# Performance work log

Measured on AMD Instinct MI355X. Metric: run time of the kernel, lower is better.

The kernel has to match this reference:

```python
import jax, jax.numpy as jnp
import numpy as np

B, L, D_MODEL = 4, 2048, 256
D_STATE, D_CONV, EXPAND = 16, 4, 2
D_INNER = EXPAND * D_MODEL          # 512
DT_RANK = (D_MODEL + 15) // 16      # 16
HORIZON = 96


def setup_inputs() -> dict:
    key = jax.random.key(0)
    ks = jax.random.split(key, 8)
    s = lambda k, shape, scale=0.02: jax.random.normal(k, shape, dtype=jnp.float32) * scale
    return {
        "x": jax.random.normal(ks[0], (B, L, D_MODEL), dtype=jnp.float32),
        "in_proj_w": s(ks[1], (2 * D_INNER, D_MODEL)),          # no bias (mamba default)
        "conv_w": s(ks[2], (D_INNER, 1, D_CONV), 0.1),          # depthwise causal conv
        "conv_b": jnp.zeros((D_INNER,), jnp.float32),
        "x_proj_w": s(ks[3], (DT_RANK + 2 * D_STATE, D_INNER)),
        "dt_proj_w": s(ks[4], (D_INNER, DT_RANK), 0.1),
        # softplus^{-1}(0.01): typical small initial dt
        "dt_proj_b": jnp.log(jnp.expm1(jnp.full((D_INNER,), 0.01, jnp.float32))),
        "A_log": jnp.log(jnp.broadcast_to(jnp.arange(1, D_STATE + 1, dtype=jnp.float32), (D_INNER, D_STATE))),
        "D_param": jnp.ones((D_INNER,), jnp.float32),
        "out_proj_w": s(ks[5], (D_MODEL, D_INNER)),
        "head_w": s(ks[6], (HORIZON, D_MODEL)),
        "head_b": jnp.zeros((HORIZON,), jnp.float32),
    }


def _silu(x):
    return x * jax.nn.sigmoid(x)


def _forward(x, in_proj_w, conv_w, conv_b, x_proj_w, dt_proj_w, dt_proj_b,
             A_log, D_param, out_proj_w, head_w, head_b):
    # in_proj -> split into conv/ssm branch and gate z
    xz = x @ in_proj_w.T                      # (B, L, 2*d_inner)
    x_in, z = jnp.split(xz, 2, axis=-1)
    # depthwise causal conv over time
    x_t = jnp.transpose(x_in, (0, 2, 1))      # (B, d_inner, L)
    x_conv = jax.lax.conv_general_dilated(
        x_t, conv_w, (1,), [(D_CONV - 1, 0)],
        feature_group_count=D_INNER, dimension_numbers=("NCH", "OIH", "NCH"))
    u = _silu(jnp.transpose(x_conv + conv_b[None, :, None], (0, 2, 1)))  # (B, L, d_inner)
    # input-dependent dt, B, C
    x_dbl = u @ x_proj_w.T
    dt, Bm, Cm = jnp.split(x_dbl, [DT_RANK, DT_RANK + D_STATE], axis=-1)
    delta = jax.nn.softplus(dt @ dt_proj_w.T + dt_proj_b)  # (B, L, d_inner)
    A = -jnp.exp(A_log)                                     # (d_inner, d_state)
    deltaA = jnp.exp(delta[..., None] * A)                  # (B, L, d_inner, d_state)
    deltaBu = delta[..., None] * Bm[:, :, None, :] * u[..., None]

    def step(h, ins):
        dA, dBu, c = ins                                    # (B,d,n),(B,d,n),(B,n)
        h = dA * h + dBu
        y = jnp.einsum("bdn,bn->bd", h, c)
        return h, y

    h0 = jnp.zeros((x.shape[0], D_INNER, D_STATE), x.dtype)
    xs = (jnp.moveaxis(deltaA, 1, 0), jnp.moveaxis(deltaBu, 1, 0), jnp.moveaxis(Cm, 1, 0))
    _, ys = jax.lax.scan(step, h0, xs)                      # (L, B, d_inner)
    y = jnp.moveaxis(ys, 0, 1) + u * D_param
    y = y * _silu(z)
    out = y @ out_proj_w.T                                  # (B, L, d_model)
    last = out[:, -1, :]
    return last @ head_w.T + head_b                         # (B, HORIZON)


def reference(x, in_proj_w, conv_w, conv_b, x_proj_w, dt_proj_w, dt_proj_b,
              A_log, D_param, out_proj_w, head_w, head_b):
    return _forward(x, in_proj_w, conv_w, conv_b, x_proj_w, dt_proj_w, dt_proj_b,
                    A_log, D_param, out_proj_w, head_w, head_b)
```

## Files before the change

kernel.cpp:

```cpp
#include <hip/hip_runtime.h>
#include <math.h>

#define BATCH 4
#define LSEQ 2048
#define BL (BATCH*LSEQ)
#define DMODEL 256
#define DINNER 512
#define NSTATE 16
#define DTRANK 16
#define NPROJ 48
#define HORIZ 96
#define NCH 32
#define TCH (LSEQ/NCH)

typedef __attribute__((ext_vector_type(8))) short short8b;
typedef __attribute__((ext_vector_type(4))) float f32x4;

__device__ __forceinline__ unsigned short f2bf(float f) {
  unsigned u = __float_as_uint(f);
  u += 0x7FFF + ((u >> 16) & 1);
  return (unsigned short)(u >> 16);
}

__global__ __launch_bounds__(256) void k_inproj(const float* __restrict__ X,
                                                const float* __restrict__ W,
                                                float* __restrict__ xinT) {
  __shared__ unsigned short sA[128][40];
  __shared__ unsigned short sB[128][40];
  const int m0 = blockIdx.x * 128;
  const int j0 = blockIdx.y * 128;
  const int tid = threadIdx.x;
  const int lane = tid & 63;
  const int wave = tid >> 6;
  const int jw = (wave & 1) * 64;
  const int mw = (wave >> 1) * 64;
  const int r  = tid >> 1;
  const int kh = (tid & 1) * 16;
  const int fl = lane & 15;
  const int fg = lane >> 4;
  const float* Asrc = &W[(size_t)(j0 + r) * DMODEL + kh];
  const float* Bsrc = &X[(size_t)(m0 + r) * DMODEL + kh];
  f32x4 acc[4][4];
  #pragma unroll
  for (int f = 0; f < 4; ++f)
    #pragma unroll
    for (int g = 0; g < 4; ++g) acc[f][g] = (f32x4){0.f, 0.f, 0.f, 0.f};
  float4 av[4], bv[4];
  #pragma unroll
  for (int q = 0; q < 4; ++q) {
    av[q] = *(const float4*)(Asrc + 4 * q);
    bv[q] = *(const float4*)(Bsrc + 4 * q);
  }
  for (int kb = 0; kb < DMODEL; kb += 32) {
    __syncthreads();
    {
      unsigned short ta[16], tb[16];
      #pragma unroll
      for (int q = 0; q < 4; ++q) {
        ta[4*q+0]=f2bf(av[q].x); ta[4*q+1]=f2bf(av[q].y); ta[4*q+2]=f2bf(av[q].z); ta[4*q+3]=f2bf(av[q].w);
        tb[4*q+0]=f2bf(bv[q].x); tb[4*q+1]=f2bf(bv[q].y); tb[4*q+2]=f2bf(bv[q].z); tb[4*q+3]=f2bf(bv[q].w);
      }
      *(short8b*)&sA[r][kh]     = *(short8b*)&ta[0];
      *(short8b*)&sA[r][kh + 8] = *(short8b*)&ta[8];
      *(short8b*)&sB[r][kh]     = *(short8b*)&tb[0];
      *(short8b*)&sB[r][kh + 8] = *(short8b*)&tb[8];
    }
    __syncthreads();
    if (kb + 32 < DMODEL) {
      #pragma unroll
      for (int q = 0; q < 4; ++q) {
        av[q] = *(const float4*)(Asrc + kb + 32 + 4 * q);
        bv[q] = *(const float4*)(Bsrc + kb + 32 + 4 * q);
      }
    }
    short8b af[4], bf[4];
    #pragma unroll
    for (int f = 0; f < 4; ++f) {
      af[f] = *(const short8b*)&sA[jw + f * 16 + fl][fg * 8];
      bf[f] = *(const short8b*)&sB[mw + f * 16 + fl][fg * 8];
    }
    #pragma unroll
    for (int f = 0; f < 4; ++f)
      #pragma unroll
      for (int g = 0; g < 4; ++g)
        acc[f][g] = __builtin_amdgcn_mfma_f32_16x16x32_bf16(af[f], bf[g], acc[f][g], 0, 0, 0);
  }
  #pragma unroll
  for (int f = 0; f < 4; ++f) {
    const int j = j0 + jw + f * 16 + fg * 4;
    #pragma unroll
    for (int g = 0; g < 4; ++g) {
      const int m = m0 + mw + g * 16 + fl;
      #pragma unroll
      for (int rg = 0; rg < 4; ++rg)
        xinT[(size_t)(j + rg) * BL + m] = acc[f][g][rg];
    }
  }
}

__global__ __launch_bounds__(256) void k_convdbl(const float* __restrict__ xinT,
                                                 const float* __restrict__ cw,
                                                 const float* __restrict__ cb,
                                                 const float* __restrict__ xpw,
                                                 const float* __restrict__ opw,
                                                 const float* __restrict__ hw,
                                                 float* __restrict__ uT,
                                                 float* __restrict__ dbl,
                                                 float* __restrict__ hwf) {
  __shared__ float sw2[48][132];
  __shared__ float su[128][33];
  const int btc = blockIdx.x;
  const int tid = threadIdx.x;
  if (btc >= 256) {
    const int fid = btc - 256;
    const int k0 = fid * 8;
    const int kk = tid & 7;
    const int t0 = tid >> 3;
    float* scratch = &sw2[0][0];
    for (int i = tid; i < 512; i += 256) {
      int m = i >> 1, half = (i & 1) << 2;
      *(float4*)&scratch[m * 8 + half] = *(const float4*)&opw[(size_t)m * DINNER + k0 + half];
    }
    __syncthreads();
    #pragma unroll
    for (int tb = 0; tb < 3; ++tb) {
      int t = tb * 32 + t0;
      const float* hr = &hw[(size_t)t * DMODEL];
      float acc = 0.f;
      #pragma unroll 8
      for (int m = 0; m < DMODEL; ++m) acc = fmaf(hr[m], scratch[m * 8 + kk], acc);
      hwf[(size_t)t * DINNER + k0 + kk] = acc;
    }
    return;
  }
  const int bt0 = btc * 32;
  const bool edge0 = ((bt0 & (LSEQ - 1)) == 0);
  const int t0 = (tid & 15) << 1;
  const int o0 = (tid >> 4) * 3;
  const int cr = tid >> 1;
  const int cc = (tid & 1) << 4;
  float acc[2][3] = {};
  for (int kp = 0; kp < 4; ++kp) {
    const int kbase = kp * 128;
    __syncthreads();
    #pragma unroll
    for (int q = 0; q < 6; ++q) {
      int idx = tid + q * 256;
      int o = idx >> 5, k4 = (idx & 31) << 2;
      *(float4*)&sw2[o][k4] = *(const float4*)&xpw[(size_t)o * DINNER + kbase + k4];
    }
    {
      const int d = kbase + cr;
      const float* xr = &xinT[(size_t)d * BL + bt0 + cc];
      float4 v0 = *(const float4*)xr;
      float4 v1 = *(const float4*)(xr + 4);
      float4 v2 = *(const float4*)(xr + 8);
      float4 v3 = *(const float4*)(xr + 12);
      bool edge = edge0 && (cc == 0);
      float p1, p2, p3;
      if (edge) { p1 = p2 = p3 = 0.f; }
      else { p1 = xr[-3]; p2 = xr[-2]; p3 = xr[-1]; }
      float4 wv = *(const float4*)&cw[d * 4];
      float bias = cb[d];
      float xv[19] = {p1, p2, p3, v0.x, v0.y, v0.z, v0.w, v1.x, v1.y, v1.z, v1.w,
                      v2.x, v2.y, v2.z, v2.w, v3.x, v3.y, v3.z, v3.w};
      float uu[16];
      #pragma unroll
      for (int c = 0; c < 16; ++c) {
        float s = bias;
        s = fmaf(wv.x, xv[c],     s);
        s = fmaf(wv.y, xv[c + 1], s);
        s = fmaf(wv.z, xv[c + 2], s);
        s = fmaf(wv.w, xv[c + 3], s);
        uu[c] = s / (1.f + __expf(-s));
      }
      #pragma unroll
      for (int q = 0; q < 4; ++q) {
        float4 w4 = make_float4(uu[4*q], uu[4*q+1], uu[4*q+2], uu[4*q+3]);
        *(float4*)&su[cr][cc + 4*q] = w4;
        *(float4*)&uT[(size_t)d * BL + bt0 + cc + 4*q] = w4;
      }
    }
    __syncthreads();
    #pragma unroll 4
    for (int kk = 0; kk < 128; ++kk) {
      float2 uv = *(const float2*)&su[kk][t0];
      float w0 = sw2[o0][kk], w1 = sw2[o0 + 1][kk], w2 = sw2[o0 + 2][kk];
      acc[0][0] = fmaf(uv.x, w0, acc[0][0]);
      acc[0][1] = fmaf(uv.x, w1, acc[0][1]);
      acc[0][2] = fmaf(uv.x, w2, acc[0][2]);
      acc[1][0] = fmaf(uv.y, w0, acc[1][0]);
      acc[1][1] = fmaf(uv.y, w1, acc[1][1]);
      acc[1][2] = fmaf(uv.y, w2, acc[1][2]);
    }
  }
  #pragma unroll
  for (int i = 0; i < 2; ++i)
    #pragma unroll
    for (int j = 0; j < 3; ++j)
      dbl[(size_t)(bt0 + t0 + i) * NPROJ + o0 + j] = acc[i][j];
}

__global__ __launch_bounds__(256) void k_scan(const float* __restrict__ uT,
                                              const float* __restrict__ dbl,
                                              const float* __restrict__ dtw,
                                              const float* __restrict__ dtb,
                                              const float* __restrict__ Alog,
                                              float* __restrict__ aprod,
                                              float* __restrict__ hacc) {
  __shared__ float sdt[64][17];
  __shared__ float sB[64][16];
  __shared__ float sdp[16][66][2];
  __shared__ float su[16][68];
  __shared__ float sdtw[16][17];
  __shared__ float sdtb[16];
  const int dblk = blockIdx.x, c = blockIdx.y, b = blockIdx.z;
  const int tid = threadIdx.x;
  const int d0 = dblk * 16;
  const int bt0 = b * LSEQ + c * TCH;
  {
    int tok = tid >> 2, q = (tid & 3) << 2;
    float4 v = *(const float4*)&dbl[(size_t)(bt0 + tok) * NPROJ + q];
    sdt[tok][q] = v.x; sdt[tok][q + 1] = v.y; sdt[tok][q + 2] = v.z; sdt[tok][q + 3] = v.w;
    float4 w = *(const float4*)&dbl[(size_t)(bt0 + tok) * NPROJ + DTRANK + q];
    *(float4*)&sB[tok][q] = w;
    int dl = tid >> 4, tq = (tid & 15) << 2;
    *(float4*)&su[dl][tq] = *(const float4*)&uT[(size_t)(d0 + dl) * BL + bt0 + tq];
    sdtw[tid >> 4][tid & 15] = dtw[(d0 + (tid >> 4)) * DTRANK + (tid & 15)];
    if (tid < 16) sdtb[tid] = dtb[d0 + tid];
  }
  __syncthreads();
  {
    int tok = tid >> 2, dl4 = (tid & 3) << 2;
    #pragma unroll
    for (int dd = 0; dd < 4; ++dd) {
      int dl = dl4 + dd;
      float a = sdtb[dl];
      #pragma unroll
      for (int r = 0; r < DTRANK; ++r) a = fmaf(sdt[tok][r], sdtw[dl][r], a);
      float dlt = (a > 20.f) ? a : log1pf(__expf(a));
      sdp[dl][tok][0] = dlt;
      sdp[dl][tok][1] = dlt * su[dl][tok];
    }
  }
  __syncthreads();
  const int dl = tid >> 4, n = tid & 15;
  const int d = d0 + dl;
  const float A = -__expf(Alog[d * NSTATE + n]);
  float ap = 1.f, h = 0.f;
  #pragma unroll 8
  for (int tt = 0; tt < TCH; ++tt) {
    float2 dp = *(const float2*)&sdp[dl][tt][0];
    float dA = __expf(dp.x * A);
    h = fmaf(dA, h, dp.y * sB[tt][n]);
    ap *= dA;
  }
  size_t off = (((size_t)b * NCH + c) * DINNER + d) * NSTATE + n;
  aprod[off] = ap;
  hacc[off] = h;
}

__global__ __launch_bounds__(256) void k_combine(const float* __restrict__ aprod,
                                                 const float* __restrict__ hacc,
                                                 const float* __restrict__ dbl,
                                                 const float* __restrict__ uT,
                                                 const float* __restrict__ Dp,
                                                 const float* __restrict__ X,
                                                 const float* __restrict__ ipw,
                                                 float* __restrict__ ybuf) {
  __shared__ float sx[DMODEL];
  const int dblk = blockIdx.x & 31, b = blockIdx.x >> 5;
  const int tid = threadIdx.x;
  const int dl = tid >> 4, n = tid & 15;
  const int d = dblk * 16 + dl;
  sx[tid] = X[((size_t)b * LSEQ + LSEQ - 1) * DMODEL + tid];
  float h = 0.f;
  for (int c = 0; c < NCH; ++c) {
    size_t off = (((size_t)b * NCH + c) * DINNER + d) * NSTATE + n;
    h = fmaf(aprod[off], h, hacc[off]);
  }
  __syncthreads();
  float zp = 0.f;
  {
    const float* zr = &ipw[(size_t)(DINNER + d) * DMODEL + (n << 4)];
    #pragma unroll
    for (int q = 0; q < 4; ++q) {
      float4 w4 = *(const float4*)&zr[q << 2];
      float4 x4 = *(const float4*)&sx[(n << 4) + (q << 2)];
      zp = fmaf(w4.x, x4.x, zp); zp = fmaf(w4.y, x4.y, zp);
      zp = fmaf(w4.z, x4.z, zp); zp = fmaf(w4.w, x4.w, zp);
    }
  }
  const int btL = b * LSEQ + LSEQ - 1;
  float Cv = dbl[(size_t)btL * NPROJ + DTRANK + NSTATE + n];
  float v = h * Cv;
  #pragma unroll
  for (int off = 1; off < 16; off <<= 1) {
    v  += __shfl_xor(v, off);
    zp += __shfl_xor(zp, off);
  }
  if (n == 0) {
    float y = v + uT[(size_t)d * BL + btL] * Dp[d];
    ybuf[b * DINNER + d] = y * zp / (1.f + __expf(-zp));
  }
}

__global__ __launch_bounds__(256) void k_out(const float* __restrict__ sy,
                                             const float* __restrict__ hwf,
                                             const float* __restrict__ hb,
                                             float* __restrict__ out) {
  const int t = blockIdx.x;
  const int b = threadIdx.x >> 6;
  const int lane = threadIdx.x & 63;
  const int k0 = lane << 3;
  const float* yr = &sy[(size_t)b * DINNER + k0];
  const float* wr = &hwf[(size_t)t * DINNER + k0];
  float4 y0 = *(const float4*)yr, y1 = *(const float4*)(yr + 4);
  float4 w0 = *(const float4*)wr, w1 = *(const float4*)(wr + 4);
  float s = y0.x * w0.x + y0.y * w0.y + y0.z * w0.z + y0.w * w0.w
          + y1.x * w1.x + y1.y * w1.y + y1.z * w1.z + y1.w * w1.w;
  #pragma unroll
  for (int off = 1; off < 64; off <<= 1) s += __shfl_xor(s, off);
  if (lane == 0) out[b * HORIZ + t] = s + hb[t];
}

extern "C" void kernel_launch(void* const* d_in, const int* in_sizes, int n_in,
                              void* d_out, int out_size, void* d_ws, size_t ws_size,
                              hipStream_t stream) {
  (void)in_sizes; (void)n_in; (void)out_size; (void)ws_size;
  const float* x    = (const float*)d_in[0];
  const float* ipw  = (const float*)d_in[1];
  const float* cw   = (const float*)d_in[2];
  const float* cb   = (const float*)d_in[3];
  const float* xpw  = (const float*)d_in[4];
  const float* dtw  = (const float*)d_in[5];
  const float* dtb  = (const float*)d_in[6];
  const float* Alog = (const float*)d_in[7];
  const float* Dp   = (const float*)d_in[8];
  const float* opw  = (const float*)d_in[9];
  const float* hw   = (const float*)d_in[10];
  const float* hb   = (const float*)d_in[11];
  float* out = (float*)d_out;
  float* ws  = (float*)d_ws;

  float* xinT  = ws;
  float* uT    = ws + 4194304;
  float* dbl   = ws + 8388608;
  float* aprod = ws + 8781824;
  float* hacc  = ws + 9830400;
  float* ybuf  = ws + 10878976;
  float* hwf   = ws + 10881024;

  k_inproj<<<dim3(64, 4), 256, 0, stream>>>(x, ipw, xinT);
  k_convdbl<<<320, 256, 0, stream>>>(xinT, cw, cb, xpw, opw, hw, uT, dbl, hwf);
  k_scan<<<dim3(32, NCH, BATCH), 256, 0, stream>>>(uT, dbl, dtw, dtb, Alog, aprod, hacc);
  k_combine<<<128, 256, 0, stream>>>(aprod, hacc, dbl, uT, Dp, x, ipw, ybuf);
  k_out<<<HORIZ, 256, 0, stream>>>(ybuf, hwf, hb, out);
}
```

Measured before the change: 77.02 us.

## Fuse in_proj GEMM with causal conv and x_proj into one front kernel

Merges the in_proj MFMA GEMM and the conv/SiLU/x_proj kernel into a single kernel. Each block computes the x_in slice for its 32 tokens plus a 16-token halo in registers, applies the depthwise causal conv through lane shuffles, and feeds u straight into the x_proj product. This removes the xinT round trip through global memory and one launch. The cost is redundant halo GEMM work per block, a double-buffered bf16 weight staging loop that syncs every k-step, and x_proj weights now rounded to bf16.

```diff
diff --git a/kernel.cpp b/kernel.cpp
--- a/kernel.cpp
+++ b/kernel.cpp
@@ -14,6 +14,7 @@
 #define TCH (LSEQ/NCH)
 
 typedef __attribute__((ext_vector_type(8))) short short8b;
+typedef __attribute__((ext_vector_type(4))) short short4b;
 typedef __attribute__((ext_vector_type(4))) float f32x4;
 
 __device__ __forceinline__ unsigned short f2bf(float f) {
@@ -21,184 +22,175 @@
   u += 0x7FFF + ((u >> 16) & 1);
   return (unsigned short)(u >> 16);
 }
-
-__global__ __launch_bounds__(256) void k_inproj(const float* __restrict__ X,
-                                                const float* __restrict__ W,
-                                                float* __restrict__ xinT) {
-  __shared__ unsigned short sA[128][40];
-  __shared__ unsigned short sB[128][40];
-  const int m0 = blockIdx.x * 128;
-  const int j0 = blockIdx.y * 128;
+__device__ __forceinline__ float bf2f(unsigned short h) {
+  return __uint_as_float(((unsigned)h) << 16);
+}
+
+__global__ __launch_bounds__(512) void k_front(const float* __restrict__ X,
+                                               const float* __restrict__ W,
+                                               const float* __restrict__ cw,
+                                               const float* __restrict__ cb,
+                                               const float* __restrict__ xpw,
+                                               const float* __restrict__ opw,
+                                               const float* __restrict__ hw,
+                                               float* __restrict__ uT,
+                                               float* __restrict__ dbl,
+                                               float* __restrict__ hwf) {
+  __shared__ unsigned short sBX[32*48*8];
+  __shared__ unsigned short sAW[2*4*128*8];
+  __shared__ float u_lds[128*36];
   const int tid = threadIdx.x;
-  const int lane = tid & 63;
-  const int wave = tid >> 6;
-  const int jw = (wave & 1) * 64;
-  const int mw = (wave >> 1) * 64;
-  const int r  = tid >> 1;
-  const int kh = (tid & 1) * 16;
-  const int fl = lane & 15;
-  const int fg = lane >> 4;
-  const float* Asrc = &W[(size_t)(j0 + r) * DMODEL + kh];
-  const float* Bsrc = &X[(size_t)(m0 + r) * DMODEL + kh];
-  f32x4 acc[4][4];
-  #pragma unroll
-  for (int f = 0; f < 4; ++f)
-    #pragma unroll
-    for (int g = 0; g < 4; ++g) acc[f][g] = (f32x4){0.f, 0.f, 0.f, 0.f};
-  float4 av[4], bv[4];
-  #pragma unroll
-  for (int q = 0; q < 4; ++q) {
-    av[q] = *(const float4*)(Asrc + 4 * q);
-    bv[q] = *(const float4*)(Bsrc + 4 * q);
-  }
-  for (int kb = 0; kb < DMODEL; kb += 32) {
-    __syncthreads();
-    {
-      unsigned short ta[16], tb[16];
-      #pragma unroll
-      for (int q = 0; q < 4; ++q) {
-        ta[4*q+0]=f2bf(av[q].x); ta[4*q+1]=f2bf(av[q].y); ta[4*q+2]=f2bf(av[q].z); ta[4*q+3]=f2bf(av[q].w);
-        tb[4*q+0]=f2bf(bv[q].x); tb[4*q+1]=f2bf(bv[q].y); tb[4*q+2]=f2bf(bv[q].z); tb[4*q+3]=f2bf(bv[q].w);
-      }
-      *(short8b*)&sA[r][kh]     = *(short8b*)&ta[0];
-      *(short8b*)&sA[r][kh + 8] = *(short8b*)&ta[8];
-      *(short8b*)&sB[r][kh]     = *(short8b*)&tb[0];
-      *(short8b*)&sB[r][kh + 8] = *(short8b*)&tb[8];
-    }
-    __syncthreads();
-    if (kb + 32 < DMODEL) {
-      #pragma unroll
-      for (int q = 0; q < 4; ++q) {
-        av[q] = *(const float4*)(Asrc + kb + 32 + 4 * q);
-        bv[q] = *(const float4*)(Bsrc + kb + 32 + 4 * q);
-      }
-    }
-    short8b af[4], bf[4];
-    #pragma unroll
-    for (int f = 0; f < 4; ++f) {
-      af[f] = *(const short8b*)&sA[jw + f * 16 + fl][fg * 8];
-      bf[f] = *(const short8b*)&sB[mw + f * 16 + fl][fg * 8];
-    }
-    #pragma unroll
-    for (int f = 0; f < 4; ++f)
-      #pragma unroll
-      for (int g = 0; g < 4; ++g)
-        acc[f][g] = __builtin_amdgcn_mfma_f32_16x16x32_bf16(af[f], bf[g], acc[f][g], 0, 0, 0);
-  }
-  #pragma unroll
-  for (int f = 0; f < 4; ++f) {
-    const int j = j0 + jw + f * 16 + fg * 4;
-    #pragma unroll
-    for (int g = 0; g < 4; ++g) {
-      const int m = m0 + mw + g * 16 + fl;
-      #pragma unroll
-      for (int rg = 0; rg < 4; ++rg)
-        xinT[(size_t)(j + rg) * BL + m] = acc[f][g][rg];
-    }
-  }
-}
-
-__global__ __launch_bounds__(256) void k_convdbl(const float* __restrict__ xinT,
-                                                 const float* __restrict__ cw,
-                                                 const float* __restrict__ cb,
-                                                 const float* __restrict__ xpw,
-                                                 const float* __restrict__ opw,
-                                                 const float* __restrict__ hw,
-                                                 float* __restrict__ uT,
-                                                 float* __restrict__ dbl,
-                                                 float* __restrict__ hwf) {
-  __shared__ float sw2[48][132];
-  __shared__ float su[128][33];
   const int btc = blockIdx.x;
-  const int tid = threadIdx.x;
   if (btc >= 256) {
     const int fid = btc - 256;
     const int k0 = fid * 8;
-    const int kk = tid & 7;
-    const int t0 = tid >> 3;
-    float* scratch = &sw2[0][0];
-    for (int i = tid; i < 512; i += 256) {
-      int m = i >> 1, half = (i & 1) << 2;
-      *(float4*)&scratch[m * 8 + half] = *(const float4*)&opw[(size_t)m * DINNER + k0 + half];
-    }
-    __syncthreads();
-    #pragma unroll
-    for (int tb = 0; tb < 3; ++tb) {
-      int t = tb * 32 + t0;
+    float* scratch = u_lds;
+    {
+      int m = tid >> 1;
+      int half = (tid & 1) << 2;
+      *(float4*)&scratch[m * 8 + half] =
+        *(const float4*)&opw[(size_t)m * DINNER + k0 + half];
+    }
+    __syncthreads();
+    for (int u = tid; u < HORIZ * 8; u += 512) {
+      int t = u >> 3, kk = u & 7;
       const float* hr = &hw[(size_t)t * DMODEL];
       float acc = 0.f;
       #pragma unroll 8
-      for (int m = 0; m < DMODEL; ++m) acc = fmaf(hr[m], scratch[m * 8 + kk], acc);
+      for (int m = 0; m < DMODEL; ++m) acc = fmaf(hr[m], scratch[m*8 + kk], acc);
       hwf[(size_t)t * DINNER + k0 + kk] = acc;
     }
     return;
   }
   const int bt0 = btc * 32;
   const bool edge0 = ((bt0 & (LSEQ - 1)) == 0);
-  const int t0 = (tid & 15) << 1;
-  const int o0 = (tid >> 4) * 3;
-  const int cr = tid >> 1;
-  const int cc = (tid & 1) << 4;
-  float acc[2][3] = {};
-  for (int kp = 0; kp < 4; ++kp) {
-    const int kbase = kp * 128;
-    __syncthreads();
+  const int lane = tid & 63;
+  const int w  = tid >> 6;
+  const int fl = lane & 15;
+  const int fg = lane >> 4;
+  for (int u = tid; u < 1536; u += 512) {
+    int tok = u >> 5, ko = u & 31;
+    int g = bt0 - 16 + tok;
+    if (g < 0) g = 0;
+    const float* xr = &X[(size_t)g * DMODEL + ko * 8];
+    float4 a = *(const float4*)xr, b = *(const float4*)(xr + 4);
+    unsigned short t8[8] = {f2bf(a.x), f2bf(a.y), f2bf(a.z), f2bf(a.w),
+                            f2bf(b.x), f2bf(b.y), f2bf(b.z), f2bf(b.w)};
+    *(short8b*)&sBX[(ko * 48 + tok) * 8] = *(short8b*)t8;
+  }
+  float facc[4] = {0.f, 0.f, 0.f, 0.f};
+  const int xo = tid >> 3;
+  const int xt = (tid & 7) * 4;
+  const int sj = tid >> 2;
+  const int sk = tid & 3;
+  for (int jc = 0; jc < 4; ++jc) {
+    const int jbase = jc * 128;
+    __syncthreads();
+    {
+      const float* wr = &W[(size_t)(jbase + sj) * DMODEL + sk * 8];
+      float4 a = *(const float4*)wr, b = *(const float4*)(wr + 4);
+      unsigned short t8[8] = {f2bf(a.x), f2bf(a.y), f2bf(a.z), f2bf(a.w),
+                              f2bf(b.x), f2bf(b.y), f2bf(b.z), f2bf(b.w)};
+      *(short8b*)&sAW[(sk * 128 + sj) * 8] = *(short8b*)t8;
+    }
+    __syncthreads();
+    f32x4 acc0 = {0,0,0,0}, acc1 = {0,0,0,0}, acc2 = {0,0,0,0};
+    for (int ks = 0; ks < 8; ++ks) {
+      const int buf = ks & 1;
+      if (ks < 7) {
+        const float* wr = &W[(size_t)(jbase + sj) * DMODEL + (ks + 1) * 32 + sk * 8];
+        float4 a = *(const float4*)wr, b = *(const float4*)(wr + 4);
+        unsigned short t8[8] = {f2bf(a.x), f2bf(a.y), f2bf(a.z), f2bf(a.w),
+                                f2bf(b.x), f2bf(b.y), f2bf(b.z), f2bf(b.w)};
+        *(short8b*)&sAW[((buf ^ 1) * 512 + sk * 128 + sj) * 8] = *(short8b*)t8;
+      }
+      short8b aw = *(short8b*)&sAW[(buf * 512 + fg * 128 + w * 16 + fl) * 8];
+      short8b x0 = *(short8b*)&sBX[((ks * 4 + fg) * 48 + fl) * 8];
+      short8b x1 = *(short8b*)&sBX[((ks * 4 + fg) * 48 + 16 + fl) * 8];
+      short8b x2 = *(short8b*)&sBX[((ks * 4 + fg) * 48 + 32 + fl) * 8];
+      acc0 = __builtin_amdgcn_mfma_f32_16x16x32_bf16(x0, aw, acc0, 0, 0, 0);
+      acc1 = __builtin_amdgcn_mfma_f32_16x16x32_bf16(x1, aw, acc1, 0, 0, 0);
+      acc2 = __builtin_amdgcn_mfma_f32_16x16x32_bf16(x2, aw, acc2, 0, 0, 0);
+      __syncthreads();
+    }
+    if (edge0) acc0 = (f32x4){0,0,0,0};
+    const int j = jbase + w * 16 + fl;
+    const float4 cwv = *(const float4*)&cw[j * 4];
+    const float cbv = cb[j];
+    float u1[4], u2[4];
+    {
+      float s3a = __shfl(acc1[3], lane - 16), s3b = __shfl(acc0[3], lane + 48);
+      float s2a = __shfl(acc1[2], lane - 16), s2b = __shfl(acc0[2], lane + 48);
+      float s1a = __shfl(acc1[1], lane - 16), s1b = __shfl(acc0[1], lane + 48);
+      float p1 = fg ? s3a : s3b, p2 = fg ? s2a : s2b, p3 = fg ? s1a : s1b;
+      float xm1[4] = {p1, acc1[0], acc1[1], acc1[2]};
+      float xm2[4] = {p2, p1, acc1[0], acc1[1]};
+      float xm3[4] = {p3, p2, p1, acc1[0]};
+      #pragma unroll
+      for (int r = 0; r < 4; ++r) {
+        float s = cbv;
+        s = fmaf(cwv.x, xm3[r], s); s = fmaf(cwv.y, xm2[r], s);
+        s = fmaf(cwv.z, xm1[r], s); s = fmaf(cwv.w, acc1[r], s);
+        u1[r] = s / (1.f + __expf(-s));
+      }
+    }
+    {
+      float s3a = __shfl(acc2[3], lane - 16), s3b = __shfl(acc1[3], lane + 48);
+      float s2a = __shfl(acc2[2], lane - 16), s2b = __shfl(acc1[2], lane + 48);
+      float s1a = __shfl(acc2[1], lane - 16), s1b = __shfl(acc1[1], lane + 48);
+      float p1 = fg ? s3a : s3b, p2 = fg ? s2a : s2b, p3 = fg ? s1a : s1b;
+      float xm1[4] = {p1, acc2[0], acc2[1], acc2[2]};
+      float xm2[4] = {p2, p1, acc2[0], acc2[1]};
+      float xm3[4] = {p3, p2, p1, acc2[0]};
+      #pragma unroll
+      for (int r = 0; r < 4; ++r) {
+        float s = cbv;
+        s = fmaf(cwv.x, xm3[r], s); s = fmaf(cwv.y, xm2[r], s);
+        s = fmaf(cwv.z, xm1[r], s); s = fmaf(cwv.w, acc2[r], s);
+        u2[r] = s / (1.f + __expf(-s));
+      }
+    }
+    {
+      const int jl = w * 16 + fl;
+      #pragma unroll
+      for (int r = 0; r < 4; ++r) {
+        u_lds[jl * 36 + fg * 4 + r]      = u1[r];
+        u_lds[jl * 36 + 16 + fg * 4 + r] = u2[r];
+      }
+    }
+    __syncthreads();
+    unsigned short* sw2 = sAW;
+    for (int u = tid; u < 1536; u += 512) {
+      int o = u >> 5, k4 = (u & 31) * 4;
+      float4 v = *(const float4*)&xpw[(size_t)o * DINNER + jbase + k4];
+      unsigned short t4[4] = {f2bf(v.x), f2bf(v.y), f2bf(v.z), f2bf(v.w)};
+      *(short4b*)&sw2[o * 136 + k4] = *(short4b*)t4;
+    }
+    {
+      const int tq = sk * 8;
+      float4 a = *(float4*)&u_lds[sj * 36 + tq];
+      float4 b = *(float4*)&u_lds[sj * 36 + tq + 4];
+      *(float4*)&uT[(size_t)(jbase + sj) * BL + bt0 + tq]     = a;
+      *(float4*)&uT[(size_t)(jbase + sj) * BL + bt0 + tq + 4] = b;
+    }
+    __syncthreads();
+    if (tid < 384) {
+      #pragma unroll 4
+      for (int k = 0; k < 128; ++k) {
+        float wv = bf2f(sw2[xo * 136 + k]);
+        float4 uv = *(float4*)&u_lds[k * 36 + xt];
+        facc[0] = fmaf(uv.x, wv, facc[0]);
+        facc[1] = fmaf(uv.y, wv, facc[1]);
+        facc[2] = fmaf(uv.z, wv, facc[2]);
+        facc[3] = fmaf(uv.w, wv, facc[3]);
+      }
+    }
+  }
+  if (tid < 384) {
     #pragma unroll
-    for (int q = 0; q < 6; ++q) {
-      int idx = tid + q * 256;
-      int o = idx >> 5, k4 = (idx & 31) << 2;
-      *(float4*)&sw2[o][k4] = *(const float4*)&xpw[(size_t)o * DINNER + kbase + k4];
-    }
-    {
-      const int d = kbase + cr;
-      const float* xr = &xinT[(size_t)d * BL + bt0 + cc];
-      float4 v0 = *(const float4*)xr;
-      float4 v1 = *(const float4*)(xr + 4);
-      float4 v2 = *(const float4*)(xr + 8);
-      float4 v3 = *(const float4*)(xr + 12);
-      bool edge = edge0 && (cc == 0);
-      float p1, p2, p3;
-      if (edge) { p1 = p2 = p3 = 0.f; }
-      else { p1 = xr[-3]; p2 = xr[-2]; p3 = xr[-1]; }
-      float4 wv = *(const float4*)&cw[d * 4];
-      float bias = cb[d];
-      float xv[19] = {p1, p2, p3, v0.x, v0.y, v0.z, v0.w, v1.x, v1.y, v1.z, v1.w,
-                      v2.x, v2.y, v2.z, v2.w, v3.x, v3.y, v3.z, v3.w};
-      float uu[16];
-      #pragma unroll
-      for (int c = 0; c < 16; ++c) {
-        float s = bias;
-        s = fmaf(wv.x, xv[c],     s);
-        s = fmaf(wv.y, xv[c + 1], s);
-        s = fmaf(wv.z, xv[c + 2], s);
-        s = fmaf(wv.w, xv[c + 3], s);
-        uu[c] = s / (1.f + __expf(-s));
-      }
-      #pragma unroll
-      for (int q = 0; q < 4; ++q) {
-        float4 w4 = make_float4(uu[4*q], uu[4*q+1], uu[4*q+2], uu[4*q+3]);
-        *(float4*)&su[cr][cc + 4*q] = w4;
-        *(float4*)&uT[(size_t)d * BL + bt0 + cc + 4*q] = w4;
-      }
-    }
-    __syncthreads();
-    #pragma unroll 4
-    for (int kk = 0; kk < 128; ++kk) {
-      float2 uv = *(const float2*)&su[kk][t0];
-      float w0 = sw2[o0][kk], w1 = sw2[o0 + 1][kk], w2 = sw2[o0 + 2][kk];
-      acc[0][0] = fmaf(uv.x, w0, acc[0][0]);
-      acc[0][1] = fmaf(uv.x, w1, acc[0][1]);
-      acc[0][2] = fmaf(uv.x, w2, acc[0][2]);
-      acc[1][0] = fmaf(uv.y, w0, acc[1][0]);
-      acc[1][1] = fmaf(uv.y, w1, acc[1][1]);
-      acc[1][2] = fmaf(uv.y, w2, acc[1][2]);
-    }
-  }
-  #pragma unroll
-  for (int i = 0; i < 2; ++i)
-    #pragma unroll
-    for (int j = 0; j < 3; ++j)
-      dbl[(size_t)(bt0 + t0 + i) * NPROJ + o0 + j] = acc[i][j];
+    for (int i = 0; i < 4; ++i)
+      dbl[(size_t)(bt0 + xt + i) * NPROJ + xo] = facc[i];
+  }
 }
 
 __global__ __launch_bounds__(256) void k_scan(const float* __restrict__ uT,
@@ -222,8 +214,8 @@
     int tok = tid >> 2, q = (tid & 3) << 2;
     float4 v = *(const float4*)&dbl[(size_t)(bt0 + tok) * NPROJ + q];
     sdt[tok][q] = v.x; sdt[tok][q + 1] = v.y; sdt[tok][q + 2] = v.z; sdt[tok][q + 3] = v.w;
-    float4 w = *(const float4*)&dbl[(size_t)(bt0 + tok) * NPROJ + DTRANK + q];
-    *(float4*)&sB[tok][q] = w;
+    float4 ww = *(const float4*)&dbl[(size_t)(bt0 + tok) * NPROJ + DTRANK + q];
+    *(float4*)&sB[tok][q] = ww;
     int dl = tid >> 4, tq = (tid & 15) << 2;
     *(float4*)&su[dl][tq] = *(const float4*)&uT[(size_t)(d0 + dl) * BL + bt0 + tq];
     sdtw[tid >> 4][tid & 15] = dtw[(d0 + (tid >> 4)) * DTRANK + (tid & 15)];
@@ -343,16 +335,14 @@
   float* out = (float*)d_out;
   float* ws  = (float*)d_ws;
 
-  float* xinT  = ws;
-  float* uT    = ws + 4194304;
-  float* dbl   = ws + 8388608;
-  float* aprod = ws + 8781824;
-  float* hacc  = ws + 9830400;
-  float* ybuf  = ws + 10878976;
-  float* hwf   = ws + 10881024;
-
-  k_inproj<<<dim3(64, 4), 256, 0, stream>>>(x, ipw, xinT);
-  k_convdbl<<<320, 256, 0, stream>>>(xinT, cw, cb, xpw, opw, hw, uT, dbl, hwf);
+  float* uT    = ws;
+  float* dbl   = ws + 4194304;
+  float* aprod = ws + 4587520;
+  float* hacc  = ws + 5636096;
+  float* ybuf  = ws + 6684672;
+  float* hwf   = ws + 6686720;
+
+  k_front<<<320, 512, 0, stream>>>(x, ipw, cw, cb, xpw, opw, hw, uT, dbl, hwf);
   k_scan<<<dim3(32, NCH, BATCH), 256, 0, stream>>>(uT, dbl, dtw, dtb, Alog, aprod, hacc);
   k_combine<<<128, 256, 0, stream>>>(aprod, hacc, dbl, uT, Dp, x, ipw, ybuf);
   k_out<<<HORIZ, 256, 0, stream>>>(ybuf, hwf, hb, out);
```

Result: slower. 79.95 us (+3.8%).
